# Kernel optimization log

Measured on AMD Instinct MI355X. Metric: run time of the kernel, lower is better.

## Reference

```python
import jax, jax.numpy as jnp
import numpy as np

N_NODES = 50000
N_EDGES = 640000
N_REL = 8
D_IN = 128
D_HID = 128
D_OUT = 64


def setup_inputs() -> dict:
    key = jax.random.key(0)
    ks = jax.random.split(key, 10)
    x = jax.random.normal(ks[0], (N_NODES, D_IN), dtype=jnp.float32)
    edge_src = jax.random.randint(ks[1], (N_EDGES,), 0, N_NODES, dtype=jnp.int32)
    edge_dst = jax.random.randint(ks[2], (N_EDGES,), 0, N_NODES, dtype=jnp.int32)
    edge_type = jax.random.randint(ks[3], (N_EDGES,), 0, N_REL, dtype=jnp.int32)
    # Glorot-ish scaling for stability
    W1 = jax.random.normal(ks[4], (N_REL, D_IN, D_HID), dtype=jnp.float32) / np.sqrt(D_IN)
    root1 = jax.random.normal(ks[5], (D_IN, D_HID), dtype=jnp.float32) / np.sqrt(D_IN)
    b1 = jnp.zeros((D_HID,), dtype=jnp.float32)
    W2 = jax.random.normal(ks[6], (N_REL, D_HID, D_OUT), dtype=jnp.float32) / np.sqrt(D_HID)
    root2 = jax.random.normal(ks[7], (D_HID, D_OUT), dtype=jnp.float32) / np.sqrt(D_HID)
    b2 = jnp.zeros((D_OUT,), dtype=jnp.float32)
    return {"x": x, "edge_src": edge_src, "edge_dst": edge_dst, "edge_type": edge_type,
            "W1": W1, "root1": root1, "b1": b1, "W2": W2, "root2": root2, "b2": b2}


def rgcn_conv(x, edge_src, edge_dst, edge_type, W, W_root, b):
    """RGCNConv with default per-relation mean aggregation + root weight + bias."""
    N = x.shape[0]
    R, _, O = W.shape
    # Transform all nodes under all relation weights once: [N, R, O]
    xW = jnp.einsum('nd,rdo->nro', x, W)
    # Gather per-edge relation-specific messages: [E, O]
    msg = xW[edge_src, edge_type]
    # Segment per (dst, relation) for mean aggregation
    seg = edge_dst.astype(jnp.int32) * R + edge_type.astype(jnp.int32)
    cnt = jax.ops.segment_sum(jnp.ones_like(edge_type, dtype=x.dtype), seg, num_segments=N * R)
    agg = jax.ops.segment_sum(msg, seg, num_segments=N * R)  # [N*R, O]
    agg = agg / jnp.maximum(cnt, 1.0)[:, None]
    rel_sum = agg.reshape(N, R, O).sum(axis=1)  # [N, O]
    return rel_sum + x @ W_root + b


def reference(x, edge_src, edge_dst, edge_type, W1, root1, b1, W2, root2, b2):
    h = rgcn_conv(x, edge_src, edge_dst, edge_type, W1, root1, b1)
    h = rgcn_conv(h, edge_src, edge_dst, edge_type, W2, root2, b2)
    return jax.nn.sigmoid(h)
```

## Files before the change

kernel.cpp:

```cpp
#include <hip/hip_runtime.h>
#include <math.h>

#define NN 50000
#define NE 640000
#define NR 8
#define SCAN_N (NN * NR)
#define SCAN_CH 2048
#define SCAN_NB ((SCAN_N + SCAN_CH - 1) / SCAN_CH)

typedef __attribute__((ext_vector_type(8))) _Float16 half8;
typedef __attribute__((ext_vector_type(8))) short short8;
typedef __attribute__((ext_vector_type(4))) float f32x4;
typedef const void __attribute__((address_space(1))) gvoid_t;
typedef void __attribute__((address_space(3))) svoid_t;

__device__ __forceinline__ unsigned short f2h(float f) {
    _Float16 h = (_Float16)f;
    return __builtin_bit_cast(unsigned short, h);
}
__device__ __forceinline__ float h2f(unsigned short u) {
    return (float)__builtin_bit_cast(_Float16, u);
}

__global__ __launch_bounds__(256) void count_kernel(const int* __restrict__ dst,
                                                    const int* __restrict__ typ,
                                                    int* __restrict__ cnt, int E) {
    int e = blockIdx.x * 256 + threadIdx.x;
    if (e < E) atomicAdd(&cnt[dst[e] * NR + typ[e]], 1);
}

__global__ __launch_bounds__(256) void inv_kernel(const int* __restrict__ cnt,
                                                  float* __restrict__ inv, int n) {
    int i = blockIdx.x * 256 + threadIdx.x;
    if (i < n) {
        int c = cnt[i];
        inv[i] = 1.0f / (float)(c > 1 ? c : 1);
    }
}

__global__ __launch_bounds__(256) void scan1_kernel(const int* __restrict__ cnt,
                                                    int* __restrict__ loc,
                                                    int* __restrict__ bsum) {
    __shared__ int s[256];
    const int t = threadIdx.x;
    const int base = blockIdx.x * SCAN_CH + t * 8;
    int v[8];
    int sum = 0;
#pragma unroll
    for (int j = 0; j < 8; ++j) {
        int idx = base + j;
        v[j] = (idx < SCAN_N) ? cnt[idx] : 0;
        sum += v[j];
    }
    s[t] = sum;
    __syncthreads();
    for (int off = 1; off < 256; off <<= 1) {
        int u = (t >= off) ? s[t - off] : 0;
        __syncthreads();
        s[t] += u;
        __syncthreads();
    }
    int run = (t == 0) ? 0 : s[t - 1];
#pragma unroll
    for (int j = 0; j < 8; ++j) {
        int idx = base + j;
        if (idx < SCAN_N) loc[idx] = run;
        run += v[j];
    }
    if (t == 255) bsum[blockIdx.x] = s[255];
}

__global__ __launch_bounds__(256) void scan2_kernel(const int* __restrict__ bsum,
                                                    int* __restrict__ boff, int nb) {
    __shared__ int s[256];
    const int t = threadIdx.x;
    s[t] = (t < nb) ? bsum[t] : 0;
    __syncthreads();
    for (int off = 1; off < 256; off <<= 1) {
        int u = (t >= off) ? s[t - off] : 0;
        __syncthreads();
        s[t] += u;
        __syncthreads();
    }
    if (t < nb) boff[t] = (t == 0) ? 0 : s[t - 1];
    if (t == nb - 1) boff[nb] = s[t];
}

__global__ __launch_bounds__(256) void scan3_kernel(int* __restrict__ rowptr,
                                                    int* __restrict__ start,
                                                    const int* __restrict__ boff, int nb) {
    const int b = blockIdx.x, t = threadIdx.x;
    const int add = boff[b];
#pragma unroll
    for (int j = 0; j < 8; ++j) {
        int idx = b * SCAN_CH + t * 8 + j;
        if (idx < SCAN_N) {
            int v = rowptr[idx] + add;
            rowptr[idx] = v;
            start[idx] = v;
        }
    }
    if (b == 0 && t == 0) rowptr[SCAN_N] = boff[nb];
}

__global__ __launch_bounds__(256) void fill_kernel(const int* __restrict__ src,
                                                   const int* __restrict__ dst,
                                                   const int* __restrict__ typ,
                                                   int* __restrict__ start,
                                                   int* __restrict__ srcrel, int E) {
    int e = blockIdx.x * 256 + threadIdx.x;
    if (e >= E) return;
    int r = typ[e];
    int pos = atomicAdd(&start[dst[e] * NR + r], 1);
    srcrel[pos] = src[e] | (r << 20);
}

__global__ __launch_bounds__(256) void cvt_kernel(const float* __restrict__ x,
                                                  unsigned short* __restrict__ xh, int n4) {
    int i = blockIdx.x * 256 + threadIdx.x;
    if (i >= n4) return;
    float4 v = ((const float4*)x)[i];
    uint2 u;
    u.x = (unsigned)f2h(v.x) | ((unsigned)f2h(v.y) << 16);
    u.y = (unsigned)f2h(v.z) | ((unsigned)f2h(v.w) << 16);
    ((uint2*)xh)[i] = u;
}

__global__ __launch_bounds__(256) void pack_b_kernel(const float* __restrict__ W,
                                                     const float* __restrict__ root,
                                                     unsigned short* __restrict__ Bt, int O) {
    int i = blockIdx.x * 256 + threadIdx.x;
    int NTOT = 9 * O;
    if (i >= NTOT * 128) return;
    int k = i & 127, n = i >> 7;
    float v = (n < 8 * O) ? W[(size_t)(n / O) * 128 * O + (size_t)k * O + (n % O)]
                          : root[(size_t)k * O + (n - 8 * O)];
    Bt[(size_t)n * 128 + k] = f2h(v);
}

template <int LDC>
__global__ __launch_bounds__(256) void gemm_xw(const unsigned short* __restrict__ A,
                                               const unsigned short* __restrict__ Bt,
                                               unsigned short* __restrict__ C) {
    __shared__ __align__(16) unsigned short As[64 * 64];
    __shared__ __align__(16) unsigned short Bs[64 * 64];
    const int t = threadIdx.x;
    const int w = t >> 6, lane = t & 63;
    const int q = lane >> 4, m = lane & 15;
    const int wr = w >> 1, wc = w & 1;
    const int bm = blockIdx.y * 64;
    const int bn = blockIdx.x * 64;

    f32x4 acc[2][2];
#pragma unroll
    for (int mb = 0; mb < 2; ++mb)
#pragma unroll
        for (int nb = 0; nb < 2; ++nb) acc[mb][nb] = (f32x4)0.f;

    const int srow = lane >> 3;
    const int gchk = (lane & 7) ^ srow;

#pragma unroll
    for (int kc = 0; kc < 2; ++kc) {
        const int k0 = kc * 64;
#pragma unroll
        for (int ii = 0; ii < 2; ++ii) {
            int i = w * 2 + ii;
            int grow = bm + i * 8 + srow;
            if (grow >= NN) grow = NN - 1;
            const unsigned short* g = A + (size_t)grow * 128 + k0 + gchk * 8;
            __builtin_amdgcn_global_load_lds((gvoid_t*)g, (svoid_t*)(As + i * 512), 16, 0, 0);
        }
#pragma unroll
        for (int ii = 0; ii < 2; ++ii) {
            int i = w * 2 + ii;
            const unsigned short* g = Bt + (size_t)(bn + i * 8 + srow) * 128 + k0 + gchk * 8;
            __builtin_amdgcn_global_load_lds((gvoid_t*)g, (svoid_t*)(Bs + i * 512), 16, 0, 0);
        }
        __syncthreads();
#pragma unroll
        for (int s = 0; s < 2; ++s) {
            const int pos8 = (((s * 4 + q) ^ (m & 7)) * 8);
            half8 af[2], bf[2];
#pragma unroll
            for (int mb = 0; mb < 2; ++mb)
                af[mb] = __builtin_bit_cast(half8,
                    *(const short8*)(As + (wr * 32 + mb * 16 + m) * 64 + pos8));
#pragma unroll
            for (int nb = 0; nb < 2; ++nb)
                bf[nb] = __builtin_bit_cast(half8,
                    *(const short8*)(Bs + (wc * 32 + nb * 16 + m) * 64 + pos8));
#pragma unroll
            for (int mb = 0; mb < 2; ++mb)
#pragma unroll
                for (int nb = 0; nb < 2; ++nb)
                    acc[mb][nb] = __builtin_amdgcn_mfma_f32_16x16x32_f16(bf[nb], af[mb],
                                                                         acc[mb][nb], 0, 0, 0);
        }
        __syncthreads();
    }

#pragma unroll
    for (int mb = 0; mb < 2; ++mb) {
        int grow = bm + wr * 32 + mb * 16 + m;
        if (grow >= NN) continue;
#pragma unroll
        for (int nb = 0; nb < 2; ++nb) {
            int col = bn + wc * 32 + nb * 16 + q * 4;
            ushort4 u;
            u.x = f2h(acc[mb][nb][0]);
            u.y = f2h(acc[mb][nb][1]);
            u.z = f2h(acc[mb][nb][2]);
            u.w = f2h(acc[mb][nb][3]);
            *(ushort4*)(C + (size_t)grow * LDC + col) = u;
        }
    }
}

template <int O, bool FINAL>
__global__ __launch_bounds__(256) void agg_kernel(const int* __restrict__ rp,
                                                  const int* __restrict__ srcrel,
                                                  const float* __restrict__ inv,
                                                  const unsigned short* __restrict__ XW,
                                                  const float* __restrict__ bias,
                                                  void* __restrict__ Hout) {
    __shared__ float sinv[4][8];
    const int slot = threadIdx.x >> 6, lane = threadIdx.x & 63;
    const int w = blockIdx.x * 4 + slot;
    if (w >= NN) return;
    if (lane < 8) sinv[slot][lane] = inv[w * NR + lane];

    const int beg = rp[w * NR], end = rp[w * NR + NR];
    constexpr int LDC2 = 9 * O / 2;

    if (O == 128) {
        const unsigned int* X2 = (const unsigned int*)XW;
        float2 acc = make_float2(0.f, 0.f);
        int i = beg;
        for (; i + 3 < end; i += 4) {
            int p0 = srcrel[i], p1 = srcrel[i + 1], p2 = srcrel[i + 2], p3 = srcrel[i + 3];
            unsigned g0 = X2[(size_t)(p0 & 0xFFFFF) * LDC2 + (((unsigned)p0) >> 20) * 64 + lane];
            unsigned g1 = X2[(size_t)(p1 & 0xFFFFF) * LDC2 + (((unsigned)p1) >> 20) * 64 + lane];
            unsigned g2 = X2[(size_t)(p2 & 0xFFFFF) * LDC2 + (((unsigned)p2) >> 20) * 64 + lane];
            unsigned g3 = X2[(size_t)(p3 & 0xFFFFF) * LDC2 + (((unsigned)p3) >> 20) * 64 + lane];
            float s0 = sinv[slot][((unsigned)p0) >> 20];
            float s1 = sinv[slot][((unsigned)p1) >> 20];
            float s2 = sinv[slot][((unsigned)p2) >> 20];
            float s3 = sinv[slot][((unsigned)p3) >> 20];
            acc.x += h2f((unsigned short)(g0 & 0xFFFFu)) * s0;
            acc.y += h2f((unsigned short)(g0 >> 16)) * s0;
            acc.x += h2f((unsigned short)(g1 & 0xFFFFu)) * s1;
            acc.y += h2f((unsigned short)(g1 >> 16)) * s1;
            acc.x += h2f((unsigned short)(g2 & 0xFFFFu)) * s2;
            acc.y += h2f((unsigned short)(g2 >> 16)) * s2;
            acc.x += h2f((unsigned short)(g3 & 0xFFFFu)) * s3;
            acc.y += h2f((unsigned short)(g3 >> 16)) * s3;
        }
        for (; i < end; ++i) {
            int p0 = srcrel[i];
            unsigned g0 = X2[(size_t)(p0 & 0xFFFFF) * LDC2 + (((unsigned)p0) >> 20) * 64 + lane];
            float s0 = sinv[slot][((unsigned)p0) >> 20];
            acc.x += h2f((unsigned short)(g0 & 0xFFFFu)) * s0;
            acc.y += h2f((unsigned short)(g0 >> 16)) * s0;
        }
        unsigned rt = X2[(size_t)w * LDC2 + 512 + lane];
        float2 bv = ((const float2*)bias)[lane];
        float vx = acc.x + h2f((unsigned short)(rt & 0xFFFFu)) + bv.x;
        float vy = acc.y + h2f((unsigned short)(rt >> 16)) + bv.y;
        ((unsigned int*)Hout)[(size_t)w * 64 + lane] =
            (unsigned)f2h(vx) | ((unsigned)f2h(vy) << 16);
    } else {
        constexpr int LDC = 9 * O;
        float acc = 0.f;
        int i = beg;
        for (; i + 3 < end; i += 4) {
            int p0 = srcrel[i], p1 = srcrel[i + 1], p2 = srcrel[i + 2], p3 = srcrel[i + 3];
            unsigned short g0 = XW[(size_t)(p0 & 0xFFFFF) * LDC + (((unsigned)p0) >> 20) * 64 + lane];
            unsigned short g1 = XW[(size_t)(p1 & 0xFFFFF) * LDC + (((unsigned)p1) >> 20) * 64 + lane];
            unsigned short g2 = XW[(size_t)(p2 & 0xFFFFF) * LDC + (((unsigned)p2) >> 20) * 64 + lane];
            unsigned short g3 = XW[(size_t)(p3 & 0xFFFFF) * LDC + (((unsigned)p3) >> 20) * 64 + lane];
            acc += h2f(g0) * sinv[slot][((unsigned)p0) >> 20];
            acc += h2f(g1) * sinv[slot][((unsigned)p1) >> 20];
            acc += h2f(g2) * sinv[slot][((unsigned)p2) >> 20];
            acc += h2f(g3) * sinv[slot][((unsigned)p3) >> 20];
        }
        for (; i < end; ++i) {
            int p0 = srcrel[i];
            unsigned short g0 = XW[(size_t)(p0 & 0xFFFFF) * LDC + (((unsigned)p0) >> 20) * 64 + lane];
            acc += h2f(g0) * sinv[slot][((unsigned)p0) >> 20];
        }
        float v = acc + h2f(XW[(size_t)w * LDC + 512 + lane]) + bias[lane];
        ((float*)Hout)[(size_t)w * 64 + lane] = 1.f / (1.f + __expf(-v));
    }
}

extern "C" void kernel_launch(void* const* d_in, const int* in_sizes, int n_in,
                              void* d_out, int out_size, void* d_ws, size_t ws_size,
                              hipStream_t stream) {
    const float* x     = (const float*)d_in[0];
    const int*   esrc  = (const int*)d_in[1];
    const int*   edst  = (const int*)d_in[2];
    const int*   etyp  = (const int*)d_in[3];
    const float* W1    = (const float*)d_in[4];
    const float* root1 = (const float*)d_in[5];
    const float* b1    = (const float*)d_in[6];
    const float* W2    = (const float*)d_in[7];
    const float* root2 = (const float*)d_in[8];
    const float* b2    = (const float*)d_in[9];
    float* out = (float*)d_out;

    char* ws = (char*)d_ws;
    unsigned short* Bt1    = (unsigned short*)ws; ws += (size_t)1152 * 128 * 2;
    unsigned short* Bt2    = (unsigned short*)ws; ws += (size_t)576 * 128 * 2;
    int*            cnt    = (int*)ws;            ws += (size_t)SCAN_N * 4;
    float*          inv    = (float*)ws;          ws += (size_t)SCAN_N * 4;
    int*            rp     = (int*)ws;            ws += (size_t)(SCAN_N + 64) * 4;
    int*            start  = (int*)ws;            ws += (size_t)SCAN_N * 4;
    int*            bsum   = (int*)ws;            ws += (size_t)256 * 4;
    int*            boff   = (int*)ws;            ws += (size_t)257 * 4;
    int*            srcrel = (int*)ws;            ws += (size_t)NE * 4;
    unsigned short* xh     = (unsigned short*)ws; ws += (size_t)NN * 128 * 2;
    unsigned short* h1b    = (unsigned short*)ws; ws += (size_t)NN * 128 * 2;
    unsigned short* xW     = (unsigned short*)ws;
    unsigned short* xW2    = xW;

    hipMemsetAsync(cnt, 0, (size_t)SCAN_N * 4, stream);
    count_kernel<<<(NE + 255) / 256, 256, 0, stream>>>(edst, etyp, cnt, NE);
    inv_kernel<<<(SCAN_N + 255) / 256, 256, 0, stream>>>(cnt, inv, SCAN_N);
    scan1_kernel<<<SCAN_NB, 256, 0, stream>>>(cnt, rp, bsum);
    scan2_kernel<<<1, 256, 0, stream>>>(bsum, boff, SCAN_NB);
    scan3_kernel<<<SCAN_NB, 256, 0, stream>>>(rp, start, boff, SCAN_NB);
    fill_kernel<<<(NE + 255) / 256, 256, 0, stream>>>(esrc, edst, etyp, start, srcrel, NE);

    cvt_kernel<<<(NN * 32 + 255) / 256, 256, 0, stream>>>(x, xh, NN * 32);
    pack_b_kernel<<<(1152 * 128 + 255) / 256, 256, 0, stream>>>(W1, root1, Bt1, 128);
    pack_b_kernel<<<(576 * 128 + 255) / 256, 256, 0, stream>>>(W2, root2, Bt2, 64);

    const int agrid = (NN + 3) / 4;
    const int gy = (NN + 63) / 64;

    gemm_xw<1152><<<dim3(1152 / 64, gy), 256, 0, stream>>>(xh, Bt1, xW);
    agg_kernel<128, false><<<agrid, 256, 0, stream>>>(rp, srcrel, inv, xW, b1, h1b);

    gemm_xw<576><<<dim3(576 / 64, gy), 256, 0, stream>>>(h1b, Bt2, xW2);
    agg_kernel<64, true><<<agrid, 256, 0, stream>>>(rp, srcrel, inv, xW2, b2, out);
}
```

Measured before the change: 337.8 us.

## Enlarge GEMM tile to 128x64 with full-K single-shot LDS staging

```diff
diff --git a/kernel.cpp b/kernel.cpp
--- a/kernel.cpp
+++ b/kernel.cpp
@@ -142,71 +142,65 @@
 __global__ __launch_bounds__(256) void gemm_xw(const unsigned short* __restrict__ A,
                                                const unsigned short* __restrict__ Bt,
                                                unsigned short* __restrict__ C) {
-    __shared__ __align__(16) unsigned short As[64 * 64];
-    __shared__ __align__(16) unsigned short Bs[64 * 64];
+    __shared__ __align__(16) unsigned short As[128 * 128];
+    __shared__ __align__(16) unsigned short Bs[64 * 128];
     const int t = threadIdx.x;
     const int w = t >> 6, lane = t & 63;
     const int q = lane >> 4, m = lane & 15;
-    const int wr = w >> 1, wc = w & 1;
-    const int bm = blockIdx.y * 64;
+    const int bm = blockIdx.y * 128;
     const int bn = blockIdx.x * 64;
 
-    f32x4 acc[2][2];
+    const int srow4 = lane >> 4, schk = lane & 15;
+
+#pragma unroll
+    for (int ii = 0; ii < 8; ++ii) {
+        int grp = w * 8 + ii;
+        int grow = bm + grp * 4 + srow4;
+        if (grow >= NN) grow = NN - 1;
+        const unsigned short* g = A + (size_t)grow * 128 + schk * 8;
+        __builtin_amdgcn_global_load_lds((gvoid_t*)g, (svoid_t*)(As + grp * 512), 16, 0, 0);
+    }
+#pragma unroll
+    for (int ii = 0; ii < 4; ++ii) {
+        int grp = w * 4 + ii;
+        const unsigned short* g = Bt + (size_t)(bn + grp * 4 + srow4) * 128 + schk * 8;
+        __builtin_amdgcn_global_load_lds((gvoid_t*)g, (svoid_t*)(Bs + grp * 512), 16, 0, 0);
+    }
+    __syncthreads();
+
+    f32x4 acc[2][4];
 #pragma unroll
     for (int mb = 0; mb < 2; ++mb)
 #pragma unroll
-        for (int nb = 0; nb < 2; ++nb) acc[mb][nb] = (f32x4)0.f;
-
-    const int srow = lane >> 3;
-    const int gchk = (lane & 7) ^ srow;
-
-#pragma unroll
-    for (int kc = 0; kc < 2; ++kc) {
-        const int k0 = kc * 64;
-#pragma unroll
-        for (int ii = 0; ii < 2; ++ii) {
-            int i = w * 2 + ii;
-            int grow = bm + i * 8 + srow;
-            if (grow >= NN) grow = NN - 1;
-            const unsigned short* g = A + (size_t)grow * 128 + k0 + gchk * 8;
-            __builtin_amdgcn_global_load_lds((gvoid_t*)g, (svoid_t*)(As + i * 512), 16, 0, 0);
-        }
-#pragma unroll
-        for (int ii = 0; ii < 2; ++ii) {
-            int i = w * 2 + ii;
-            const unsigned short* g = Bt + (size_t)(bn + i * 8 + srow) * 128 + k0 + gchk * 8;
-            __builtin_amdgcn_global_load_lds((gvoid_t*)g, (svoid_t*)(Bs + i * 512), 16, 0, 0);
-        }
-        __syncthreads();
-#pragma unroll
-        for (int s = 0; s < 2; ++s) {
-            const int pos8 = (((s * 4 + q) ^ (m & 7)) * 8);
-            half8 af[2], bf[2];
-#pragma unroll
-            for (int mb = 0; mb < 2; ++mb)
-                af[mb] = __builtin_bit_cast(half8,
-                    *(const short8*)(As + (wr * 32 + mb * 16 + m) * 64 + pos8));
-#pragma unroll
-            for (int nb = 0; nb < 2; ++nb)
-                bf[nb] = __builtin_bit_cast(half8,
-                    *(const short8*)(Bs + (wc * 32 + nb * 16 + m) * 64 + pos8));
-#pragma unroll
-            for (int mb = 0; mb < 2; ++mb)
-#pragma unroll
-                for (int nb = 0; nb < 2; ++nb)
-                    acc[mb][nb] = __builtin_amdgcn_mfma_f32_16x16x32_f16(bf[nb], af[mb],
-                                                                         acc[mb][nb], 0, 0, 0);
-        }
-        __syncthreads();
+        for (int nb = 0; nb < 4; ++nb) acc[mb][nb] = (f32x4)0.f;
+
+#pragma unroll
+    for (int s = 0; s < 4; ++s) {
+        const int pos = s * 32 + q * 8;
+        half8 af[2], bf[4];
+#pragma unroll
+        for (int mb = 0; mb < 2; ++mb)
+            af[mb] = __builtin_bit_cast(half8,
+                *(const short8*)(As + (w * 32 + mb * 16 + m) * 128 + pos));
+#pragma unroll
+        for (int nb = 0; nb < 4; ++nb)
+            bf[nb] = __builtin_bit_cast(half8,
+                *(const short8*)(Bs + (nb * 16 + m) * 128 + pos));
+#pragma unroll
+        for (int mb = 0; mb < 2; ++mb)
+#pragma unroll
+            for (int nb = 0; nb < 4; ++nb)
+                acc[mb][nb] = __builtin_amdgcn_mfma_f32_16x16x32_f16(bf[nb], af[mb],
+                                                                     acc[mb][nb], 0, 0, 0);
     }
 
 #pragma unroll
     for (int mb = 0; mb < 2; ++mb) {
-        int grow = bm + wr * 32 + mb * 16 + m;
+        int grow = bm + w * 32 + mb * 16 + m;
         if (grow >= NN) continue;
 #pragma unroll
-        for (int nb = 0; nb < 2; ++nb) {
-            int col = bn + wc * 32 + nb * 16 + q * 4;
+        for (int nb = 0; nb < 4; ++nb) {
+            int col = bn + nb * 16 + q * 4;
             ushort4 u;
             u.x = f2h(acc[mb][nb][0]);
             u.y = f2h(acc[mb][nb][1]);
@@ -337,7 +331,7 @@
     pack_b_kernel<<<(576 * 128 + 255) / 256, 256, 0, stream>>>(W2, root2, Bt2, 64);
 
     const int agrid = (NN + 3) / 4;
-    const int gy = (NN + 63) / 64;
+    const int gy = (NN + 127) / 128;
 
     gemm_xw<1152><<<dim3(1152 / 64, gy), 256, 0, stream>>>(xh, Bt1, xW);
     agg_kernel<128, false><<<agrid, 256, 0, stream>>>(rp, srcrel, inv, xW, b1, h1b);
```

Result: no change. 336.1 us (-0.5%).
